# Performance work log

Measured on AMD Instinct MI355X. Metric: run time of the kernel, lower is better.

The kernel has to match this reference:

```python
import jax, jax.numpy as jnp
import numpy as np

HIDDEN = 2048
N_HEADS = 16
N_KV_HEADS = 4
HEAD_DIM = HIDDEN // N_HEADS  # 128
BATCH = 1
SEQ = 2048
EPS = 1e-6


def _rms_norm(x, scale, eps=EPS):
    var = jnp.mean(jnp.square(x), axis=-1, keepdims=True)
    return x * jax.lax.rsqrt(var + eps) * scale


def _rotate_half(x):
    x1, x2 = jnp.split(x, 2, axis=-1)
    return jnp.concatenate((-x2, x1), axis=-1)


def setup_inputs() -> dict:
    key = jax.random.key(0)
    ks = jax.random.split(key, 8)
    hidden_states = jax.random.normal(ks[0], (BATCH, SEQ, HIDDEN), dtype=jnp.float32)
    # causal mask, broadcastable over [B, H, S, S]
    attention_mask = jnp.tril(jnp.ones((SEQ, SEQ), dtype=bool))[None, None, :, :]
    # standard RoPE tables, broadcastable against [B, S, H, D]
    inv_freq = 1.0 / (10000.0 ** (np.arange(0, HEAD_DIM, 2, dtype=np.float32) / HEAD_DIM))
    t = np.arange(SEQ, dtype=np.float32)
    freqs = np.outer(t, inv_freq)                      # [S, D/2]
    emb = np.concatenate([freqs, freqs], axis=-1)      # [S, D]
    cos = jnp.asarray(np.cos(emb))[:, None, :]         # [S, 1, D]
    sin = jnp.asarray(np.sin(emb))[:, None, :]
    s = 1.0 / np.sqrt(HIDDEN)
    Wq = jax.random.normal(ks[1], (HIDDEN, N_HEADS * HEAD_DIM), dtype=jnp.float32) * s
    Wk = jax.random.normal(ks[2], (HIDDEN, N_KV_HEADS * HEAD_DIM), dtype=jnp.float32) * s
    Wv = jax.random.normal(ks[3], (HIDDEN, N_KV_HEADS * HEAD_DIM), dtype=jnp.float32) * s
    Wo = jax.random.normal(ks[4], (HIDDEN, HIDDEN), dtype=jnp.float32) * s
    q_norm_scale = jnp.ones((HEAD_DIM,), dtype=jnp.float32)
    k_norm_scale = jnp.ones((HEAD_DIM,), dtype=jnp.float32)
    last_norm_scale = jnp.ones((HIDDEN,), dtype=jnp.float32)
    return {
        "hidden_states": hidden_states,
        "cos": cos,
        "sin": sin,
        "Wq": Wq,
        "Wk": Wk,
        "Wv": Wv,
        "Wo": Wo,
        "q_norm_scale": q_norm_scale,
        "k_norm_scale": k_norm_scale,
        "last_norm_scale": last_norm_scale,
        "attention_mask": attention_mask,
    }


def reference(hidden_states, cos, sin, Wq, Wk, Wv, Wo,
              q_norm_scale, k_norm_scale, last_norm_scale, attention_mask):
    B, S, _ = hidden_states.shape
    q = (hidden_states @ Wq).reshape(B, S, N_HEADS, HEAD_DIM)
    k = (hidden_states @ Wk).reshape(B, S, N_KV_HEADS, HEAD_DIM)
    v = (hidden_states @ Wv).reshape(B, S, N_KV_HEADS, HEAD_DIM)
    # per-head RMSNorm on Q/K
    q = _rms_norm(q, q_norm_scale)
    k = _rms_norm(k, k_norm_scale)
    # RoPE (cos/sin broadcast [S,1,D] -> [B,S,H,D])
    q = q * cos + _rotate_half(q) * sin
    k = k * cos + _rotate_half(k) * sin
    # GQA expansion
    groups = N_HEADS // N_KV_HEADS
    if groups > 1:
        k = jnp.repeat(k, groups, axis=2)
        v = jnp.repeat(v, groups, axis=2)
    out = jax.nn.dot_product_attention(q, k, v, mask=attention_mask)  # [B,S,H,D]
    out = out.reshape(B, S, HIDDEN) @ Wo
    return _rms_norm(out, last_norm_scale)
```

## Files before the change

### kernel.cpp

```cpp
#include <hip/hip_runtime.h>

typedef unsigned short u16;
typedef unsigned int u32;

#define S 2048
#define HID 2048
#define NH 16
#define NKV 4
#define D 128
#define QKVP 3072
#define QSCALE (0.08838834764831845f * 1.4426950408889634f)
#define NEG_INF -3.0e38f

typedef __attribute__((ext_vector_type(8))) short short8;
typedef __attribute__((ext_vector_type(4))) float f32x4;

__device__ __forceinline__ float bf2f(u16 u) {
  union { u32 i; float f; } c; c.i = ((u32)u) << 16; return c.f;
}
__device__ __forceinline__ u16 f2bf(float f) {
  union { float f; u32 i; } c; c.f = f;
  u32 x = c.i;
  u32 r = x + 0x7fffu + ((x >> 16) & 1u);
  return (u16)(r >> 16);
}

#if __has_builtin(__builtin_amdgcn_exp2f)
__device__ __forceinline__ float exp2_hw(float x) { return __builtin_amdgcn_exp2f(x); }
#else
__device__ __forceinline__ float exp2_hw(float x) { return exp2f(x); }
#endif

__device__ __forceinline__ u32 cvt_pk_bf16(float a, float b) {
  u32 r;
  asm("v_cvt_pk_bf16_f32 %0, %1, %2" : "=v"(r) : "v"(a), "v"(b));
  return r;
}

__device__ __forceinline__ void gload16(const u16* g, u16* l) {
  __builtin_amdgcn_global_load_lds(
      (const __attribute__((address_space(1))) u32*)g,
      (__attribute__((address_space(3))) u32*)l, 16, 0, 0);
}

__global__ __launch_bounds__(256) void k_cvt(const float* __restrict__ src,
                                             u16* __restrict__ dst) {
  int i = (blockIdx.x * 256 + threadIdx.x) * 8;
  float4 v0 = *(const float4*)(src + i);
  float4 v1 = *(const float4*)(src + i + 4);
  ushort4 w0, w1;
  w0.x = f2bf(v0.x); w0.y = f2bf(v0.y); w0.z = f2bf(v0.z); w0.w = f2bf(v0.w);
  w1.x = f2bf(v1.x); w1.y = f2bf(v1.y); w1.z = f2bf(v1.z); w1.w = f2bf(v1.w);
  *(ushort4*)(dst + i) = w0;
  *(ushort4*)(dst + i + 4) = w1;
}

__device__ __forceinline__ void transpose_body(const float* __restrict__ src,
                                               u16* __restrict__ dst,
                                               int N, int K, int nt, int kt,
                                               int t) {
  __shared__ float T[64][65];
#pragma unroll
  for (int it = 0; it < 4; ++it) {
    int r = it * 16 + (t >> 4), c = (t & 15) * 4;
    float4 v = *(const float4*)(src + (size_t)(kt + r) * N + nt + c);
    T[r][c] = v.x; T[r][c + 1] = v.y; T[r][c + 2] = v.z; T[r][c + 3] = v.w;
  }
  __syncthreads();
#pragma unroll
  for (int it = 0; it < 2; ++it) {
    int n = it * 32 + (t >> 3), k8 = (t & 7) * 8;
    ushort4 w0, w1;
    w0.x = f2bf(T[k8 + 0][n]); w0.y = f2bf(T[k8 + 1][n]);
    w0.z = f2bf(T[k8 + 2][n]); w0.w = f2bf(T[k8 + 3][n]);
    w1.x = f2bf(T[k8 + 4][n]); w1.y = f2bf(T[k8 + 5][n]);
    w1.z = f2bf(T[k8 + 6][n]); w1.w = f2bf(T[k8 + 7][n]);
    *(ushort4*)(dst + (size_t)(nt + n) * K + kt + k8) = w0;
    *(ushort4*)(dst + (size_t)(nt + n) * K + kt + k8 + 4) = w1;
  }
}

__global__ __launch_bounds__(256) void k_transpose(const float* __restrict__ src,
                                                   u16* __restrict__ dst,
                                                   int N, int K) {
  transpose_body(src, dst, N, K, blockIdx.x * 64, blockIdx.y * 64, threadIdx.x);
}

__global__ __launch_bounds__(256) void k_transpose_qkv(const float* __restrict__ Wq,
                                                       const float* __restrict__ Wk,
                                                       const float* __restrict__ Wv,
                                                       u16* __restrict__ WT) {
  const int bx = blockIdx.x;
  const float* src; u16* dst; int N, nt;
  if (bx < 32)      { src = Wq; dst = WT;                    N = 2048; nt = bx * 64; }
  else if (bx < 40) { src = Wk; dst = WT + 2048ull * 2048;   N = 512;  nt = (bx - 32) * 64; }
  else              { src = Wv; dst = WT + 2560ull * 2048;   N = 512;  nt = (bx - 40) * 64; }
  transpose_body(src, dst, N, 2048, nt, blockIdx.y * 64, threadIdx.x);
}

__global__ __launch_bounds__(256) void k_vt(const u16* __restrict__ QKV,
                                            u16* __restrict__ Vt) {
  __shared__ u16 T[64][66];
  const int t = threadIdx.x;
  const int s0 = blockIdx.x * 64, d0 = blockIdx.y * 64;
#pragma unroll
  for (int it = 0; it < 4; ++it) {
    int r = it * 16 + (t >> 4), c = (t & 15) * 4;
    ushort4 v = *(const ushort4*)(QKV + (size_t)(s0 + r) * QKVP + 2560 + d0 + c);
    T[r][c] = v.x; T[r][c + 1] = v.y; T[r][c + 2] = v.z; T[r][c + 3] = v.w;
  }
  __syncthreads();
#pragma unroll
  for (int it = 0; it < 4; ++it) {
    int dd = it * 16 + (t >> 4), sc = (t & 15) * 4;
    ushort4 w;
    w.x = T[sc + 0][dd]; w.y = T[sc + 1][dd];
    w.z = T[sc + 2][dd]; w.w = T[sc + 3][dd];
    *(ushort4*)(Vt + (size_t)(d0 + dd) * S + s0 + sc) = w;
  }
}

__global__ __launch_bounds__(256) void k_gemm_mfma(const u16* __restrict__ A,
                                                   const u16* __restrict__ BT,
                                                   void* __restrict__ Cout,
                                                   int N, int K, int out_bf16) {
  __shared__ __align__(16) u16 As[2][128 * 64];
  __shared__ __align__(16) u16 Bs[2][128 * 64];
  const int t = threadIdx.x, w = t >> 6, lane = t & 63;
  const int l15 = lane & 15, quad = lane >> 4;
  const int m0 = blockIdx.y * 128, n0 = blockIdx.x * 128;
  const int wr = w >> 1, wc = w & 1;

  const int srow = lane >> 3;
  const int schunk = (lane & 7) ^ srow;
  const u16* Agb = A + (size_t)(m0 + w * 8 + srow) * K + schunk * 8;
  const u16* Bgb = BT + (size_t)(n0 + w * 8 + srow) * K + schunk * 8;

  f32x4 acc[4][4];
#pragma unroll
  for (int i = 0; i < 4; ++i)
#pragma unroll
    for (int j = 0; j < 4; ++j) acc[i][j] = (f32x4){0.f, 0.f, 0.f, 0.f};

  auto STAGE = [&](int k0, int b) {
#pragma unroll
    for (int it = 0; it < 4; ++it) {
      gload16(Agb + (size_t)it * 32 * K + k0, &As[b][(w * 8 + it * 32) * 64]);
      gload16(Bgb + (size_t)it * 32 * K + k0, &Bs[b][(w * 8 + it * 32) * 64]);
    }
  };

  STAGE(0, 0);
  __syncthreads();
  int cur = 0;
  for (int k0 = 0; k0 < K; k0 += 64) {
    if (k0 + 64 < K) STAGE(k0 + 64, cur ^ 1);

    short8 af[4][2], bf[4][2];
#pragma unroll
    for (int i = 0; i < 4; ++i)
#pragma unroll
      for (int k2 = 0; k2 < 2; ++k2) {
        int ch = (k2 * 4 + quad) ^ (l15 & 7);
        af[i][k2] = *(const short8*)&As[cur][(wr * 64 + i * 16 + l15) * 64 + ch * 8];
        bf[i][k2] = *(const short8*)&Bs[cur][(wc * 64 + i * 16 + l15) * 64 + ch * 8];
      }
#pragma unroll
    for (int k2 = 0; k2 < 2; ++k2)
#pragma unroll
      for (int i = 0; i < 4; ++i)
#pragma unroll
        for (int j = 0; j < 4; ++j)
          acc[i][j] = __builtin_amdgcn_mfma_f32_16x16x32_bf16(af[i][k2], bf[j][k2], acc[i][j], 0, 0, 0);

    __syncthreads();
    cur ^= 1;
  }

  if (out_bf16) {
    u16* C = (u16*)Cout;
#pragma unroll
    for (int i = 0; i < 4; ++i)
#pragma unroll
      for (int j = 0; j < 4; ++j) {
        int col = n0 + wc * 64 + j * 16 + l15;
#pragma unroll
        for (int r = 0; r < 4; ++r)
          C[(size_t)(m0 + wr * 64 + i * 16 + quad * 4 + r) * N + col] = f2bf(acc[i][j][r]);
      }
  } else {
    float* C = (float*)Cout;
#pragma unroll
    for (int i = 0; i < 4; ++i)
#pragma unroll
      for (int j = 0; j < 4; ++j) {
        int col = n0 + wc * 64 + j * 16 + l15;
#pragma unroll
        for (int r = 0; r < 4; ++r)
          C[(size_t)(m0 + wr * 64 + i * 16 + quad * 4 + r) * N + col] = acc[i][j][r];
      }
  }
}

__global__ __launch_bounds__(128) void k_norm_rope(u16* __restrict__ QKV,
                                                   const float* __restrict__ qsc,
                                                   const float* __restrict__ ksc,
                                                   const float* __restrict__ cosp,
                                                   const float* __restrict__ sinp) {
  const int s = blockIdx.x, hh = blockIdx.y, d = threadIdx.x;
  u16* row; const float* sc; float scale;
  if (hh < NH) { row = QKV + (size_t)s * QKVP + hh * D;            sc = qsc; scale = QSCALE; }
  else         { row = QKV + (size_t)s * QKVP + 2048 + (hh - NH) * D; sc = ksc; scale = 1.0f; }
  float x = bf2f(row[d]);
  float v = x * x;
#pragma unroll
  for (int o = 32; o; o >>= 1) v += __shfl_xor(v, o, 64);
  __shared__ float red[2];
  if ((d & 63) == 0) red[d >> 6] = v;
  __syncthreads();
  float var = (red[0] + red[1]) * (1.0f / 128.0f);
  float rinv = rsqrtf(var + 1e-6f) * scale;
  float xn = x * rinv * sc[d];
  __shared__ float sh[D];
  sh[d] = xn;
  __syncthreads();
  float rot = (d < 64) ? -sh[d + 64] : sh[d - 64];
  row[d] = f2bf(xn * cosp[s * D + d] + rot * sinp[s * D + d]);
}

#define KVB 32
#define KP 128
#define PTP 72

__global__ __launch_bounds__(256) void k_flash(const u16* __restrict__ QKV,
                                               const u16* __restrict__ Vt,
                                               u16* __restrict__ O) {
  const int h = blockIdx.y, g = h >> 2;
  const int qt = (h < 8) ? (31 - (int)blockIdx.x) : (int)blockIdx.x;
  const int t = threadIdx.x;
  const int w = t >> 6, lane = t & 63, l15 = lane & 15, quad = lane >> 4;

  __shared__ __align__(16) u16 Klds[4][2][KVB * KP];
  __shared__ __align__(16) u16 Pt[4][16 * PTP];

  u16* Kw[2] = {&Klds[w][0][0], &Klds[w][1][0]};

  const int qrow = qt * 64 + w * 16 + l15;

  short8 qf[4];
  {
    const u16* qp = QKV + (size_t)qrow * QKVP + h * D + quad * 8;
#pragma unroll
    for (int c = 0; c < 4; ++c) qf[c] = *(const short8*)(qp + c * 32);
  }

  float m = NEG_INF, l = 0.f;
  f32x4 oacc[8];
#pragma unroll
  for (int nc = 0; nc < 8; ++nc) oacc[nc] = (f32x4){0.f, 0.f, 0.f, 0.f};

  const int nt = ((qt * 64 + w * 16 + 15) >> 5) + 1;

  auto KLOAD = [&](int j0, u16* dst) {
#pragma unroll
    for (int it = 0; it < 8; ++it) {
      int rl = it * 4 + quad;
      int gchunk = l15 ^ (rl & 7);
      const u16* gp = QKV + (size_t)(j0 + rl) * QKVP + 2048 + g * D + gchunk * 8;
      gload16(gp, dst + (it * 4) * KP);
    }
  };

  KLOAD(0, Kw[0]);
  for (int jt = 0; jt < nt; ++jt) {
    const u16* kb = Kw[jt & 1];
    if (jt + 1 < nt) {
      KLOAD((jt + 1) * KVB, Kw[(jt & 1) ^ 1]);
      asm volatile("s_waitcnt vmcnt(8)" ::: "memory");
    } else {
      asm volatile("s_waitcnt vmcnt(0)" ::: "memory");
    }

    const int j0 = jt * KVB;
    const u16* vbase = Vt + (size_t)g * D * S + j0;

    short8 vf[8];
#pragma unroll
    for (int nc = 0; nc < 8; ++nc)
      vf[nc] = *(const short8*)(vbase + (size_t)(nc * 16 + l15) * S + quad * 8);

    f32x4 sa[2];
#pragma unroll
    for (int sub = 0; sub < 2; ++sub) {
      f32x4 acc = {0.f, 0.f, 0.f, 0.f};
#pragma unroll
      for (int c = 0; c < 4; ++c) {
        int ch = (c * 4 + quad) ^ (l15 & 7);
        short8 kf = *(const short8*)&kb[(sub * 16 + l15) * KP + ch * 8];
        acc = __builtin_amdgcn_mfma_f32_16x16x32_bf16(kf, qf[c], acc, 0, 0, 0);
      }
      sa[sub] = acc;
    }

    if (jt == nt - 1) {
#pragma unroll
      for (int sub = 0; sub < 2; ++sub) {
        int keyb = j0 + sub * 16 + quad * 4;
#pragma unroll
        for (int r = 0; r < 4; ++r)
          if (keyb + r > qrow) sa[sub][r] = NEG_INF;
      }
    }

    float tmax = sa[0][0];
#pragma unroll
    for (int sub = 0; sub < 2; ++sub)
#pragma unroll
      for (int r = 0; r < 4; ++r) tmax = fmaxf(tmax, sa[sub][r]);
    tmax = fmaxf(tmax, __shfl_xor(tmax, 16, 64));
    tmax = fmaxf(tmax, __shfl_xor(tmax, 32, 64));
    if (jt == 0 || !__all(tmax - m <= 8.f)) {
      float mn = (jt == 0) ? tmax : fmaxf(m, tmax);
      float alpha = (jt == 0) ? 0.f : exp2_hw(m - mn);
      m = mn;
      l *= alpha;
#pragma unroll
      for (int nc = 0; nc < 8; ++nc) {
        oacc[nc][0] *= alpha; oacc[nc][1] *= alpha;
        oacc[nc][2] *= alpha; oacc[nc][3] *= alpha;
      }
    }
    float rs = 0.f;
#pragma unroll
    for (int sub = 0; sub < 2; ++sub) {
      float p0 = exp2_hw(sa[sub][0] - m);
      float p1 = exp2_hw(sa[sub][1] - m);
      float p2 = exp2_hw(sa[sub][2] - m);
      float p3 = exp2_hw(sa[sub][3] - m);
      rs += (p0 + p1) + (p2 + p3);
      u32 lo = cvt_pk_bf16(p0, p1);
      u32 hi = cvt_pk_bf16(p2, p3);
      *(uint2*)&Pt[w][l15 * PTP + sub * 16 + quad * 4] = make_uint2(lo, hi);
    }
    rs += __shfl_xor(rs, 16, 64);
    rs += __shfl_xor(rs, 32, 64);
    l += rs;

    {
      short8 pf = *(const short8*)&Pt[w][l15 * PTP + quad * 8];
#pragma unroll
      for (int nc = 0; nc < 8; ++nc)
        oacc[nc] = __builtin_amdgcn_mfma_f32_16x16x32_bf16(vf[nc], pf, oacc[nc], 0, 0, 0);
    }
  }

  float inv = 1.0f / l;
  u16* orow = O + (size_t)qrow * HID + h * D;
#pragma unroll
  for (int nc = 0; nc < 8; ++nc) {
    ushort4 wv;
    wv.x = f2bf(oacc[nc][0] * inv); wv.y = f2bf(oacc[nc][1] * inv);
    wv.z = f2bf(oacc[nc][2] * inv); wv.w = f2bf(oacc[nc][3] * inv);
    *(ushort4*)(orow + nc * 16 + quad * 4) = wv;
  }
}

__device__ __forceinline__ float blockSum256(float v, float* red, int t) {
#pragma unroll
  for (int o = 32; o; o >>= 1) v += __shfl_xor(v, o, 64);
  if ((t & 63) == 0) red[t >> 6] = v;
  __syncthreads();
  v = red[0] + red[1] + red[2] + red[3];
  __syncthreads();
  return v;
}

__global__ __launch_bounds__(256) void k_fnorm(const float* __restrict__ X,
                                               const float* __restrict__ sc,
                                               float* __restrict__ out) {
  const int s = blockIdx.x, t = threadIdx.x;
  const float* row = X + (size_t)s * HID;
  float4 r0 = *(const float4*)(row + t * 8);
  float4 r1 = *(const float4*)(row + t * 8 + 4);
  float x[8] = {r0.x, r0.y, r0.z, r0.w, r1.x, r1.y, r1.z, r1.w};
  float ss = 0.f;
#pragma unroll
  for (int ii = 0; ii < 8; ++ii) ss += x[ii] * x[ii];
  __shared__ float red[4];
  float tot = blockSum256(ss, red, t);
  float rinv = rsqrtf(tot * (1.0f / 2048.0f) + 1e-6f);
  float4 s0 = *(const float4*)(sc + t * 8);
  float4 s1 = *(const float4*)(sc + t * 8 + 4);
  float4 w0 = make_float4(x[0] * rinv * s0.x, x[1] * rinv * s0.y,
                          x[2] * rinv * s0.z, x[3] * rinv * s0.w);
  float4 w1 = make_float4(x[4] * rinv * s1.x, x[5] * rinv * s1.y,
                          x[6] * rinv * s1.z, x[7] * rinv * s1.w);
  *(float4*)(out + (size_t)s * HID + t * 8) = w0;
  *(float4*)(out + (size_t)s * HID + t * 8 + 4) = w1;
}

extern "C" void kernel_launch(void* const* d_in, const int* in_sizes, int n_in,
                              void* d_out, int out_size, void* d_ws, size_t ws_size,
                              hipStream_t stream) {
  const float* hidden = (const float*)d_in[0];
  const float* cosp   = (const float*)d_in[1];
  const float* sinp   = (const float*)d_in[2];
  const float* Wq     = (const float*)d_in[3];
  const float* Wk     = (const float*)d_in[4];
  const float* Wv     = (const float*)d_in[5];
  const float* Wo     = (const float*)d_in[6];
  const float* qsc    = (const float*)d_in[7];
  const float* ksc    = (const float*)d_in[8];
  const float* lsc    = (const float*)d_in[9];
  float* out = (float*)d_out;

  char* ws = (char*)d_ws;
  u16*   Hb  = (u16*)(ws);
  u16*   WoT = (u16*)(ws);
  u16*   WT  = (u16*)(ws + (8ull << 20));
  u16*   An  = (u16*)(ws + (8ull << 20));
  u16*   QKV = (u16*)(ws + (20ull << 20));
  float* Ob  = (float*)(ws + (20ull << 20));
  u16*   Vtb = (u16*)(ws + (32ull << 20));

  k_cvt<<<S * HID / (256 * 8), 256, 0, stream>>>(hidden, Hb);
  k_transpose_qkv<<<dim3(48, 32), 256, 0, stream>>>(Wq, Wk, Wv, WT);
  k_gemm_mfma<<<dim3(24, 16), 256, 0, stream>>>(Hb, WT, QKV, QKVP, 2048, 1);
  k_transpose<<<dim3(32, 32), 256, 0, stream>>>(Wo, WoT, 2048, 2048);
  k_norm_rope<<<dim3(S, NH + NKV), 128, 0, stream>>>(QKV, qsc, ksc, cosp, sinp);
  k_vt<<<dim3(32, 8), 256, 0, stream>>>(QKV, Vtb);
  k_flash<<<dim3(32, NH), 256, 0, stream>>>(QKV, Vtb, An);
  k_gemm_mfma<<<dim3(16, 16), 256, 0, stream>>>(An, WoT, Ob, 2048, 2048, 0);
  k_fnorm<<<S, 256, 0, stream>>>(Ob, lsc, out);
}
```

Measured before the change: 307.5 us.

## Read K directly from global memory and widen flash key tile to 64

Drops the per-wave LDS double-buffered K staging with async loads and instead loads K fragments straight from global memory into registers. The key tile per iteration grows from 32 to 64, so the loop count is set to qt+1 and two V fragment sets and two P fragments feed the PV MFMAs. This removes LDS traffic and the waitcnt synchronisation and halves the loop iterations. In exchange, K is read uncoalesced with a long row stride, register pressure rises from the doubled V fragments, and every wave now runs to the 64-row tile bound, so some extra fully-masked work is done.

Result: slower. 334.3 us (+8.7%).

```diff
diff --git a/kernel.cpp b/kernel.cpp
--- a/kernel.cpp
+++ b/kernel.cpp
@@ -228,8 +228,6 @@
   row[d] = f2bf(xn * cosp[s * D + d] + rot * sinp[s * D + d]);
 }
 
-#define KVB 32
-#define KP 128
 #define PTP 72
 
 __global__ __launch_bounds__(256) void k_flash(const u16* __restrict__ QKV,
@@ -240,10 +238,7 @@
   const int t = threadIdx.x;
   const int w = t >> 6, lane = t & 63, l15 = lane & 15, quad = lane >> 4;
 
-  __shared__ __align__(16) u16 Klds[4][2][KVB * KP];
   __shared__ __align__(16) u16 Pt[4][16 * PTP];
-
-  u16* Kw[2] = {&Klds[w][0][0], &Klds[w][1][0]};
 
   const int qrow = qt * 64 + w * 16 + l15;
 
@@ -259,52 +254,39 @@
 #pragma unroll
   for (int nc = 0; nc < 8; ++nc) oacc[nc] = (f32x4){0.f, 0.f, 0.f, 0.f};
 
-  const int nt = ((qt * 64 + w * 16 + 15) >> 5) + 1;
-
-  auto KLOAD = [&](int j0, u16* dst) {
-#pragma unroll
-    for (int it = 0; it < 8; ++it) {
-      int rl = it * 4 + quad;
-      int gchunk = l15 ^ (rl & 7);
-      const u16* gp = QKV + (size_t)(j0 + rl) * QKVP + 2048 + g * D + gchunk * 8;
-      gload16(gp, dst + (it * 4) * KP);
-    }
-  };
-
-  KLOAD(0, Kw[0]);
+  const int nt = qt + 1;
+  const u16* Kb = QKV + 2048 + (size_t)g * D;
+  const u16* Vb = Vt + (size_t)g * D * S;
+
   for (int jt = 0; jt < nt; ++jt) {
-    const u16* kb = Kw[jt & 1];
-    if (jt + 1 < nt) {
-      KLOAD((jt + 1) * KVB, Kw[(jt & 1) ^ 1]);
-      asm volatile("s_waitcnt vmcnt(8)" ::: "memory");
-    } else {
-      asm volatile("s_waitcnt vmcnt(0)" ::: "memory");
-    }
-
-    const int j0 = jt * KVB;
-    const u16* vbase = Vt + (size_t)g * D * S + j0;
-
-    short8 vf[8];
+    const int j0 = jt * 64;
+
+    short8 vf0[8];
 #pragma unroll
     for (int nc = 0; nc < 8; ++nc)
-      vf[nc] = *(const short8*)(vbase + (size_t)(nc * 16 + l15) * S + quad * 8);
-
-    f32x4 sa[2];
-#pragma unroll
-    for (int sub = 0; sub < 2; ++sub) {
+      vf0[nc] = *(const short8*)(Vb + (size_t)(nc * 16 + l15) * S + j0 + quad * 8);
+
+    f32x4 sa[4];
+#pragma unroll
+    for (int sub = 0; sub < 4; ++sub) {
+      const u16* krow = Kb + (size_t)(j0 + sub * 16 + l15) * QKVP + quad * 8;
       f32x4 acc = {0.f, 0.f, 0.f, 0.f};
 #pragma unroll
       for (int c = 0; c < 4; ++c) {
-        int ch = (c * 4 + quad) ^ (l15 & 7);
-        short8 kf = *(const short8*)&kb[(sub * 16 + l15) * KP + ch * 8];
+        short8 kf = *(const short8*)(krow + c * 32);
         acc = __builtin_amdgcn_mfma_f32_16x16x32_bf16(kf, qf[c], acc, 0, 0, 0);
       }
       sa[sub] = acc;
     }
 
+    short8 vf1[8];
+#pragma unroll
+    for (int nc = 0; nc < 8; ++nc)
+      vf1[nc] = *(const short8*)(Vb + (size_t)(nc * 16 + l15) * S + j0 + 32 + quad * 8);
+
     if (jt == nt - 1) {
 #pragma unroll
-      for (int sub = 0; sub < 2; ++sub) {
+      for (int sub = 0; sub < 4; ++sub) {
         int keyb = j0 + sub * 16 + quad * 4;
 #pragma unroll
         for (int r = 0; r < 4; ++r)
@@ -314,7 +296,7 @@
 
     float tmax = sa[0][0];
 #pragma unroll
-    for (int sub = 0; sub < 2; ++sub)
+    for (int sub = 0; sub < 4; ++sub)
 #pragma unroll
       for (int r = 0; r < 4; ++r) tmax = fmaxf(tmax, sa[sub][r]);
     tmax = fmaxf(tmax, __shfl_xor(tmax, 16, 64));
@@ -332,7 +314,7 @@
     }
     float rs = 0.f;
 #pragma unroll
-    for (int sub = 0; sub < 2; ++sub) {
+    for (int sub = 0; sub < 4; ++sub) {
       float p0 = exp2_hw(sa[sub][0] - m);
       float p1 = exp2_hw(sa[sub][1] - m);
       float p2 = exp2_hw(sa[sub][2] - m);
@@ -347,10 +329,14 @@
     l += rs;
 
     {
-      short8 pf = *(const short8*)&Pt[w][l15 * PTP + quad * 8];
+      short8 pf0 = *(const short8*)&Pt[w][l15 * PTP + quad * 8];
+      short8 pf1 = *(const short8*)&Pt[w][l15 * PTP + 32 + quad * 8];
 #pragma unroll
       for (int nc = 0; nc < 8; ++nc)
-        oacc[nc] = __builtin_amdgcn_mfma_f32_16x16x32_bf16(vf[nc], pf, oacc[nc], 0, 0, 0);
+        oacc[nc] = __builtin_amdgcn_mfma_f32_16x16x32_bf16(vf0[nc], pf0, oacc[nc], 0, 0, 0);
+#pragma unroll
+      for (int nc = 0; nc < 8; ++nc)
+        oacc[nc] = __builtin_amdgcn_mfma_f32_16x16x32_bf16(vf1[nc], pf1, oacc[nc], 0, 0, 0);
     }
   }
 
```
